# Kernel tuning notes

Measured on AMD Instinct MI355X. Metric: run time of the kernel, lower is better.

The kernel has to match this reference:

```python
import jax, jax.numpy as jnp
import numpy as np
import math

SCALED = True
SUBSEQUENT_MASK = True
B, SQ, SK, D, DV = 8, 2048, 2048, 1024, 1024


def _build_mask(query_lens, key_lens, sq, sk, causal):
    # (B, Sq, Sk) boolean validity mask: rows >= q_len and cols >= k_len are masked.
    qm = jnp.arange(sq)[None, :, None] < query_lens[:, None, None]
    km = jnp.arange(sk)[None, None, :] < key_lens[:, None, None]
    mask = qm & km
    if causal:
        mask = mask & (jnp.arange(sk)[None, None, :] <= jnp.arange(sq)[None, :, None])
    return mask


def _masked_softmax(scores, mask):
    # Stable masked softmax; fully-masked rows yield exactly 0 (matches the
    # original's NaN -> 0 replacement) without producing NaNs.
    neg = jnp.finfo(scores.dtype).min
    s = jnp.where(mask, scores, neg)
    m = jnp.max(s, axis=-1, keepdims=True)
    e = jnp.where(mask, jnp.exp(s - m), jnp.zeros((), scores.dtype))
    denom = jnp.sum(e, axis=-1, keepdims=True)
    return e / jnp.where(denom == 0, jnp.ones((), scores.dtype), denom)


def setup_inputs() -> dict:
    key = jax.random.key(0)
    kq, kk, kv, kql, kkl = jax.random.split(key, 5)
    return {
        "queries": jax.random.normal(kq, (B, SQ, D), dtype=jnp.float32),
        "keys": jax.random.normal(kk, (B, SK, D), dtype=jnp.float32),
        "values": jax.random.normal(kv, (B, SK, DV), dtype=jnp.float32),
        "query_lens": jax.random.randint(kql, (B,), 1, SQ + 1),
        "key_lens": jax.random.randint(kkl, (B,), 1, SK + 1),
    }


def reference(queries, keys, values, query_lens, key_lens):
    # scores: (B, Sq, Sk)
    scores = jnp.einsum("bqd,bkd->bqk", queries, keys)
    if SCALED:
        scores = scores / math.sqrt(queries.shape[2])
    mask = _build_mask(query_lens, key_lens, queries.shape[1], keys.shape[1], SUBSEQUENT_MASK)
    weights = _masked_softmax(scores, mask)
    context = jnp.einsum("bqk,bkv->bqv", weights, values)
    return (context, weights)
```

## Files before the change

kernel.cpp:

```cpp
#include <hip/hip_runtime.h>
#include <hip/hip_bf16.h>

#define B_   8
#define SQ_  2048
#define SK_  2048
#define D_   1024
#define DV_  1024

typedef __bf16 bf16;
typedef __attribute__((ext_vector_type(4))) __bf16 bf16x4;
typedef __attribute__((ext_vector_type(8))) __bf16 bf16x8;
typedef __attribute__((ext_vector_type(4))) float  f32x4;

typedef const __attribute__((address_space(1))) void* gptr1;
typedef __attribute__((address_space(3))) void*       lptr3;

__device__ __forceinline__ void gload16(const void* g, void* l) {
    __builtin_amdgcn_global_load_lds((gptr1)g, (lptr3)l, 16, 0, 0);
}

__global__ __launch_bounds__(256)
void convert_kernel(const float* __restrict__ A, const float* __restrict__ Bm,
                    bf16* __restrict__ dA, bf16* __restrict__ dB)
{
    const float* src = blockIdx.y ? Bm : A;
    bf16*        dst = blockIdx.y ? dB : dA;
    size_t i = ((size_t)blockIdx.x * 256 + threadIdx.x) * 8;
    float4 v0 = *(const float4*)(src + i);
    float4 v1 = *(const float4*)(src + i + 4);
    bf16x8 o = { (bf16)v0.x, (bf16)v0.y, (bf16)v0.z, (bf16)v0.w,
                 (bf16)v1.x, (bf16)v1.y, (bf16)v1.z, (bf16)v1.w };
    *(bf16x8*)(dst + i) = o;
}

__global__ __launch_bounds__(256)
void convVT_kernel(const float* __restrict__ V, bf16* __restrict__ VT)
{
    const int b  = blockIdx.z;
    const int k0 = blockIdx.x * 64;
    const int n0 = blockIdx.y * 64;
    __shared__ bf16 T[64][72];

    const int tid = threadIdx.x;
    #pragma unroll
    for (int i = 0; i < 4; ++i) {
        int s  = tid + i * 256;
        int r  = s >> 4;
        int c4 = (s & 15) << 2;
        float4 v = *(const float4*)(V + ((size_t)b * SK_ + (k0 + r)) * DV_ + n0 + c4);
        T[r][c4 + 0] = (bf16)v.x;
        T[r][c4 + 1] = (bf16)v.y;
        T[r][c4 + 2] = (bf16)v.z;
        T[r][c4 + 3] = (bf16)v.w;
    }
    __syncthreads();
    #pragma unroll
    for (int i = 0; i < 2; ++i) {
        int s  = tid + i * 256;
        int n  = s >> 3;
        int c8 = (s & 7) << 3;
        bf16x8 o;
        #pragma unroll
        for (int j = 0; j < 8; ++j) o[j] = T[c8 + j][n];
        *(bf16x8*)(VT + ((size_t)b * DV_ + (n0 + n)) * SK_ + k0 + c8) = o;
    }
}

__global__ __launch_bounds__(512, 4)
void scores_bf_kernel(const bf16* __restrict__ Qbf, const bf16* __restrict__ Kbf,
                      const int* __restrict__ qlens, const int* __restrict__ klens,
                      float* __restrict__ Wout)
{
    const int b  = blockIdx.z;
    const int q0 = blockIdx.y * 128;
    const int k0 = blockIdx.x * 128;
    if (k0 > q0 + 127) return;
    const int qlen = qlens[b], klen = klens[b];
    if (q0 >= qlen || k0 >= klen) return;

    __shared__ __align__(16) bf16 Qs[2][128][64];
    __shared__ __align__(16) bf16 Ks[2][128][64];

    const int tid  = threadIdx.x;
    const int lane = tid & 63;
    const int w    = tid >> 6;
    const int wq   = w >> 1, wk = w & 1;

    const bf16* Qb = Qbf + (size_t)b * SQ_ * D_ + (size_t)q0 * D_;
    const bf16* Kb = Kbf + (size_t)b * SK_ * D_ + (size_t)k0 * D_;

    const int r0 = tid >> 3;
    const int c0 = (tid & 7) << 3;

    auto stage = [&](int buf, int d0) {
        gload16(Qb + (size_t)r0 * D_ + d0 + c0,        &Qs[buf][r0][c0]);
        gload16(Qb + (size_t)(r0 + 64) * D_ + d0 + c0, &Qs[buf][r0 + 64][c0]);
        gload16(Kb + (size_t)r0 * D_ + d0 + c0,        &Ks[buf][r0][c0]);
        gload16(Kb + (size_t)(r0 + 64) * D_ + d0 + c0, &Ks[buf][r0 + 64][c0]);
    };

    f32x4 acc[2][4] = {};

    stage(0, 0);
    __syncthreads();

    for (int it = 0; it < 16; ++it) {
        const int cur = it & 1;
        if (it < 15) stage(cur ^ 1, (it + 1) * 64);
        #pragma unroll
        for (int kk = 0; kk < 2; ++kk) {
            const int koff = kk * 32 + ((lane >> 4) << 3);
            bf16x8 a[2], bb[4];
            #pragma unroll
            for (int m = 0; m < 2; ++m)
                a[m] = *(const bf16x8*)&Qs[cur][32 * wq + 16 * m + (lane & 15)][koff];
            #pragma unroll
            for (int n = 0; n < 4; ++n)
                bb[n] = *(const bf16x8*)&Ks[cur][64 * wk + 16 * n + (lane & 15)][koff];
            #pragma unroll
            for (int m = 0; m < 2; ++m)
                #pragma unroll
                for (int n = 0; n < 4; ++n)
                    acc[m][n] = __builtin_amdgcn_mfma_f32_16x16x32_bf16(a[m], bb[n], acc[m][n], 0, 0, 0);
        }
        __syncthreads();
    }

    float* Wb = Wout + (size_t)b * SQ_ * SK_;
    const int rb = q0 + 32 * wq + ((lane >> 4) << 2);
    const int cb = k0 + 64 * wk + (lane & 15);
    #pragma unroll
    for (int m = 0; m < 2; ++m)
        #pragma unroll
        for (int n = 0; n < 4; ++n)
            #pragma unroll
            for (int r = 0; r < 4; ++r)
                Wb[(size_t)(rb + 16 * m + r) * SK_ + (cb + 16 * n)] = acc[m][n][r] * 0.03125f;
}

__global__ __launch_bounds__(256)
void softmax_kernel(const int* __restrict__ qlens, const int* __restrict__ klens,
                    float* __restrict__ W, bf16* __restrict__ Wbf)
{
    const int bq = blockIdx.x;
    const int b  = bq >> 11;
    const int q  = bq & 2047;
    const int qlen = qlens[b], klen = klens[b];
    int kmax = 0;
    if (q < qlen) kmax = min(klen, q + 1);

    float4* row = (float4*)(W + (size_t)bq * SK_);
    const int tid = threadIdx.x;

    float4 x[2];
    float m = -INFINITY;
    #pragma unroll
    for (int i = 0; i < 2; ++i) {
        int v4 = tid + i * 256;
        int kb = v4 << 2;
        if (kb < kmax) x[i] = row[v4];
        else           x[i] = make_float4(-INFINITY, -INFINITY, -INFINITY, -INFINITY);
        float* xe = (float*)&x[i];
        #pragma unroll
        for (int e = 0; e < 4; ++e) {
            if (kb + e >= kmax) xe[e] = -INFINITY;
            m = fmaxf(m, xe[e]);
        }
    }
    #pragma unroll
    for (int off = 32; off > 0; off >>= 1) m = fmaxf(m, __shfl_xor(m, off, 64));
    __shared__ float red[4];
    if ((tid & 63) == 0) red[tid >> 6] = m;
    __syncthreads();
    m = fmaxf(fmaxf(red[0], red[1]), fmaxf(red[2], red[3]));
    __syncthreads();

    float sum = 0.f;
    #pragma unroll
    for (int i = 0; i < 2; ++i) {
        float* xe = (float*)&x[i];
        #pragma unroll
        for (int e = 0; e < 4; ++e) {
            float ev = (xe[e] == -INFINITY) ? 0.f : __expf(xe[e] - m);
            xe[e] = ev;
            sum += ev;
        }
    }
    #pragma unroll
    for (int off = 32; off > 0; off >>= 1) sum += __shfl_xor(sum, off, 64);
    if ((tid & 63) == 0) red[tid >> 6] = sum;
    __syncthreads();
    sum = red[0] + red[1] + red[2] + red[3];

    const float inv = (sum > 0.f) ? (1.f / sum) : 0.f;
    #pragma unroll
    for (int i = 0; i < 2; ++i) {
        float* xe = (float*)&x[i];
        float4 o = { xe[0] * inv, xe[1] * inv, xe[2] * inv, xe[3] * inv };
        row[tid + i * 256] = o;
        if (Wbf) {
            bf16x4 ob = { (bf16)o.x, (bf16)o.y, (bf16)o.z, (bf16)o.w };
            *(bf16x4*)(Wbf + (size_t)bq * SK_ + ((size_t)(tid + i * 256) << 2)) = ob;
        }
    }
}

__global__ __launch_bounds__(512, 4)
void context_bf_kernel(const bf16* __restrict__ Wbf, const bf16* __restrict__ VT,
                       const int* __restrict__ qlens, const int* __restrict__ klens,
                       float* __restrict__ Out)
{
    const int b  = blockIdx.z;
    const int q0 = blockIdx.y * 128;
    const int n0 = blockIdx.x * 128;
    const int tid  = threadIdx.x;
    const int qlen = qlens[b];

    float* Ob = Out + (size_t)b * SQ_ * DV_;
    if (q0 >= qlen) {
        float4 z = make_float4(0.f, 0.f, 0.f, 0.f);
        #pragma unroll
        for (int i = 0; i < 8; ++i) {
            int s  = tid + i * 512;
            int r  = s >> 5;
            int c4 = (s & 31) << 2;
            *(float4*)(Ob + (size_t)(q0 + r) * DV_ + n0 + c4) = z;
        }
        return;
    }

    const int klen = klens[b];
    const int kend = min(q0 + 128, (klen + 63) & ~63);
    const int nk   = kend >> 6;

    __shared__ __align__(16) bf16 Ws[2][128][64];
    __shared__ __align__(16) bf16 Vs[2][128][64];

    const int lane = tid & 63;
    const int w    = tid >> 6;
    const int wq   = w >> 1, wn = w & 1;

    const bf16* Wb = Wbf + (size_t)b * SQ_ * SK_ + (size_t)q0 * SK_;
    const bf16* Vb = VT  + (size_t)b * DV_ * SK_ + (size_t)n0 * SK_;

    const int r0 = tid >> 3;
    const int c0 = (tid & 7) << 3;

    auto stage = [&](int buf, int kk0) {
        gload16(Wb + (size_t)r0 * SK_ + kk0 + c0,        &Ws[buf][r0][c0]);
        gload16(Wb + (size_t)(r0 + 64) * SK_ + kk0 + c0, &Ws[buf][r0 + 64][c0]);
        gload16(Vb + (size_t)r0 * SK_ + kk0 + c0,        &Vs[buf][r0][c0]);
        gload16(Vb + (size_t)(r0 + 64) * SK_ + kk0 + c0, &Vs[buf][r0 + 64][c0]);
    };

    f32x4 acc[2][4] = {};

    stage(0, 0);
    __syncthreads();

    for (int it = 0; it < nk; ++it) {
        const int cur = it & 1;
        if (it + 1 < nk) stage(cur ^ 1, (it + 1) * 64);
        #pragma unroll
        for (int kk = 0; kk < 2; ++kk) {
            const int koff = kk * 32 + ((lane >> 4) << 3);
            bf16x8 a[2], bb[4];
            #pragma unroll
            for (int m = 0; m < 2; ++m)
                a[m] = *(const bf16x8*)&Ws[cur][32 * wq + 16 * m + (lane & 15)][koff];
            #pragma unroll
            for (int n = 0; n < 4; ++n)
                bb[n] = *(const bf16x8*)&Vs[cur][64 * wn + 16 * n + (lane & 15)][koff];
            #pragma unroll
            for (int m = 0; m < 2; ++m)
                #pragma unroll
                for (int n = 0; n < 4; ++n)
                    acc[m][n] = __builtin_amdgcn_mfma_f32_16x16x32_bf16(a[m], bb[n], acc[m][n], 0, 0, 0);
        }
        __syncthreads();
    }

    const int rb = q0 + 32 * wq + ((lane >> 4) << 2);
    const int cb = n0 + 64 * wn + (lane & 15);
    #pragma unroll
    for (int m = 0; m < 2; ++m)
        #pragma unroll
        for (int n = 0; n < 4; ++n)
            #pragma unroll
            for (int r = 0; r < 4; ++r)
                Ob[(size_t)(rb + 16 * m + r) * DV_ + (cb + 16 * n)] = acc[m][n][r];
}

__global__ __launch_bounds__(512, 4)
void scores_kernel(const float* __restrict__ Q, const float* __restrict__ K,
                   const int* __restrict__ qlens, const int* __restrict__ klens,
                   float* __restrict__ Wout)
{
    const int b  = blockIdx.z;
    const int q0 = blockIdx.y * 128;
    const int k0 = blockIdx.x * 128;
    if (k0 > q0 + 127) return;
    const int qlen = qlens[b], klen = klens[b];
    if (q0 >= qlen || k0 >= klen) return;

    __shared__ __align__(16) bf16 Qs[2][128][72];
    __shared__ __align__(16) bf16 Ks[2][128][72];

    const int tid  = threadIdx.x;
    const int lane = tid & 63;
    const int w    = tid >> 6;
    const int wq   = w >> 1, wk = w & 1;

    const float* Qb = Q + (size_t)b * SQ_ * D_;
    const float* Kb = K + (size_t)b * SK_ * D_;

    float4 qreg[4], kreg[4];
    int srow[4], sc4[4];
    #pragma unroll
    for (int i = 0; i < 4; ++i) {
        int s = tid + i * 512;
        srow[i] = s >> 4;
        sc4[i]  = (s & 15) << 2;
    }

    auto load_tile = [&](int d0) {
        #pragma unroll
        for (int i = 0; i < 4; ++i) {
            qreg[i] = *(const float4*)(Qb + (size_t)(q0 + srow[i]) * D_ + d0 + sc4[i]);
            kreg[i] = *(const float4*)(Kb + (size_t)(k0 + srow[i]) * D_ + d0 + sc4[i]);
        }
    };
    auto store_tile = [&](int buf) {
        #pragma unroll
        for (int i = 0; i < 4; ++i) {
            bf16x4 qb = { (bf16)qreg[i].x, (bf16)qreg[i].y, (bf16)qreg[i].z, (bf16)qreg[i].w };
            bf16x4 kb = { (bf16)kreg[i].x, (bf16)kreg[i].y, (bf16)kreg[i].z, (bf16)kreg[i].w };
            *(bf16x4*)&Qs[buf][srow[i]][sc4[i]] = qb;
            *(bf16x4*)&Ks[buf][srow[i]][sc4[i]] = kb;
        }
    };

    f32x4 acc[2][4] = {};
    load_tile(0);
    store_tile(0);
    __syncthreads();

    for (int it = 0; it < 16; ++it) {
        const int cur = it & 1;
        if (it < 15) load_tile((it + 1) * 64);
        #pragma unroll
        for (int kk = 0; kk < 2; ++kk) {
            const int koff = kk * 32 + ((lane >> 4) << 3);
            bf16x8 a[2], bb[4];
            #pragma unroll
            for (int m = 0; m < 2; ++m)
                a[m] = *(const bf16x8*)&Qs[cur][32 * wq + 16 * m + (lane & 15)][koff];
            #pragma unroll
            for (int n = 0; n < 4; ++n)
                bb[n] = *(const bf16x8*)&Ks[cur][64 * wk + 16 * n + (lane & 15)][koff];
            #pragma unroll
            for (int m = 0; m < 2; ++m)
                #pragma unroll
                for (int n = 0; n < 4; ++n)
                    acc[m][n] = __builtin_amdgcn_mfma_f32_16x16x32_bf16(a[m], bb[n], acc[m][n], 0, 0, 0);
        }
        if (it < 15) store_tile(1 - cur);
        __syncthreads();
    }

    float* Wb = Wout + (size_t)b * SQ_ * SK_;
    const int rb = q0 + 32 * wq + ((lane >> 4) << 2);
    const int cb = k0 + 64 * wk + (lane & 15);
    #pragma unroll
    for (int m = 0; m < 2; ++m)
        #pragma unroll
        for (int n = 0; n < 4; ++n)
            #pragma unroll
            for (int r = 0; r < 4; ++r)
                Wb[(size_t)(rb + 16 * m + r) * SK_ + (cb + 16 * n)] = acc[m][n][r] * 0.03125f;
}

__global__ __launch_bounds__(512, 4)
void context_kernel(const float* __restrict__ W, const float* __restrict__ V,
                    const int* __restrict__ klens, float* __restrict__ Out)
{
    const int b  = blockIdx.z;
    const int q0 = blockIdx.y * 128;
    const int n0 = blockIdx.x * 128;
    const int klen = klens[b];
    const int kend = min(q0 + 128, (klen + 63) & ~63);
    const int nk   = kend >> 6;

    __shared__ __align__(16) bf16 Ws[2][128][72];
    __shared__ __align__(16) bf16 Vs[2][128][72];

    const int tid  = threadIdx.x;
    const int lane = tid & 63;
    const int w    = tid >> 6;
    const int wq   = w >> 1, wn = w & 1;

    const float* Wb = W + (size_t)b * SQ_ * SK_;
    const float* Vb = V + (size_t)b * SK_ * DV_;

    float4 wreg[4];
    float  vreg[2][8];
    int srow[4], sc4[4], vn[2], voct[2];
    #pragma unroll
    for (int i = 0; i < 4; ++i) {
        int s = tid + i * 512;
        srow[i] = s >> 4;
        sc4[i]  = (s & 15) << 2;
    }
    #pragma unroll
    for (int i = 0; i < 2; ++i) {
        int t = tid + i * 512;
        vn[i]   = t & 127;
        voct[i] = t >> 7;
    }

    auto load_tile = [&](int kk0) {
        #pragma unroll
        for (int i = 0; i < 4; ++i)
            wreg[i] = *(const float4*)(Wb + (size_t)(q0 + srow[i]) * SK_ + kk0 + sc4[i]);
        #pragma unroll
        for (int i = 0; i < 2; ++i)
            #pragma unroll
            for (int j = 0; j < 8; ++j)
                vreg[i][j] = Vb[(size_t)(kk0 + voct[i] * 8 + j) * DV_ + n0 + vn[i]];
    };
    auto store_tile = [&](int buf) {
        #pragma unroll
        for (int i = 0; i < 4; ++i) {
            bf16x4 wb = { (bf16)wreg[i].x, (bf16)wreg[i].y, (bf16)wreg[i].z, (bf16)wreg[i].w };
            *(bf16x4*)&Ws[buf][srow[i]][sc4[i]] = wb;
        }
        #pragma unroll
        for (int i = 0; i < 2; ++i) {
            bf16x8 vb = { (bf16)vreg[i][0], (bf16)vreg[i][1], (bf16)vreg[i][2], (bf16)vreg[i][3],
                          (bf16)vreg[i][4], (bf16)vreg[i][5], (bf16)vreg[i][6], (bf16)vreg[i][7] };
            *(bf16x8*)&Vs[buf][vn[i]][voct[i] * 8] = vb;
        }
    };

    f32x4 acc[2][4] = {};
    load_tile(0);
    store_tile(0);
    __syncthreads();

    for (int it = 0; it < nk; ++it) {
        const int cur = it & 1;
        if (it + 1 < nk) load_tile((it + 1) * 64);
        #pragma unroll
        for (int kk = 0; kk < 2; ++kk) {
            const int koff = kk * 32 + ((lane >> 4) << 3);
            bf16x8 a[2], bb[4];
            #pragma unroll
            for (int m = 0; m < 2; ++m)
                a[m] = *(const bf16x8*)&Ws[cur][32 * wq + 16 * m + (lane & 15)][koff];
            #pragma unroll
            for (int n = 0; n < 4; ++n)
                bb[n] = *(const bf16x8*)&Vs[cur][64 * wn + 16 * n + (lane & 15)][koff];
            #pragma unroll
            for (int m = 0; m < 2; ++m)
                #pragma unroll
                for (int n = 0; n < 4; ++n)
                    acc[m][n] = __builtin_amdgcn_mfma_f32_16x16x32_bf16(a[m], bb[n], acc[m][n], 0, 0, 0);
        }
        if (it + 1 < nk) store_tile(1 - cur);
        __syncthreads();
    }

    float* Ob = Out + (size_t)b * SQ_ * DV_;
    const int rb = q0 + 32 * wq + ((lane >> 4) << 2);
    const int cb = n0 + 64 * wn + (lane & 15);
    #pragma unroll
    for (int m = 0; m < 2; ++m)
        #pragma unroll
        for (int n = 0; n < 4; ++n)
            #pragma unroll
            for (int r = 0; r < 4; ++r)
                Ob[(size_t)(rb + 16 * m + r) * DV_ + (cb + 16 * n)] = acc[m][n][r];
}

extern "C" void kernel_launch(void* const* d_in, const int* in_sizes, int n_in,
                              void* d_out, int out_size, void* d_ws, size_t ws_size,
                              hipStream_t stream) {
    (void)in_sizes; (void)n_in; (void)out_size;
    const float* Q     = (const float*)d_in[0];
    const float* K     = (const float*)d_in[1];
    const float* V     = (const float*)d_in[2];
    const int*   qlens = (const int*)d_in[3];
    const int*   klens = (const int*)d_in[4];

    float* ctx = (float*)d_out;
    float* wts = ctx + (size_t)B_ * SQ_ * DV_;

    const size_t nQ = (size_t)B_ * SQ_ * D_;
    const size_t nK = (size_t)B_ * SK_ * D_;
    const size_t nV = (size_t)B_ * SK_ * DV_;
    const size_t nW = (size_t)B_ * SQ_ * SK_;
    const size_t ws_need = (nQ + nK + nV + nW) * sizeof(bf16);

    if (d_ws && ws_size >= ws_need) {
        bf16* qbf = (bf16*)d_ws;
        bf16* kbf = qbf + nQ;
        bf16* vbt = kbf + nK;
        bf16* wbf = vbt + nV;

        convert_kernel<<<dim3((unsigned)(nQ / (256 * 8)), 2), 256, 0, stream>>>(Q, K, qbf, kbf);
        convVT_kernel<<<dim3(SK_ / 64, DV_ / 64, B_), 256, 0, stream>>>(V, vbt);

        dim3 g1(SK_ / 128, SQ_ / 128, B_);
        scores_bf_kernel<<<g1, 512, 0, stream>>>(qbf, kbf, qlens, klens, wts);

        softmax_kernel<<<dim3(B_ * SQ_), 256, 0, stream>>>(qlens, klens, wts, wbf);

        dim3 g3(DV_ / 128, SQ_ / 128, B_);
        context_bf_kernel<<<g3, 512, 0, stream>>>(wbf, vbt, qlens, klens, ctx);
    } else {
        dim3 g1(SK_ / 128, SQ_ / 128, B_);
        scores_kernel<<<g1, 512, 0, stream>>>(Q, K, qlens, klens, wts);

        softmax_kernel<<<dim3(B_ * SQ_), 256, 0, stream>>>(qlens, klens, wts, (bf16*)nullptr);

        dim3 g3(DV_ / 128, SQ_ / 128, B_);
        context_kernel<<<g3, 512, 0, stream>>>(wts, V, klens, ctx);
    }
}
```

Measured before the change: 492.8 us.

## Fuse exp into QK kernel and defer softmax normalization to context epilogue

The separate scores and softmax passes are replaced by an attnP kernel that computes QK^T tiles, applies the mask and exp without subtracting a row max, writes unnormalized bf16 probabilities, and accumulates row sums via atomics. A normW kernel then writes the normalized fp32 weights from the bf16 buffer, and the context kernel scales its output by the inverse row sum. The goal is to cut the fp32 score write and read round trip and the separate softmax pass. In exchange, the QK grid becomes 512 blocks of 64-row tiles that loop over key tiles, which lowers parallelism and reloads Q for each key tile. Dropping the max subtraction risks overflow for inputs with large scores, and the fp32 weights are now rounded through bf16.

```diff
diff --git a/kernel.cpp b/kernel.cpp
--- a/kernel.cpp
+++ b/kernel.cpp
@@ -21,8 +21,15 @@
 
 __global__ __launch_bounds__(256)
 void convert_kernel(const float* __restrict__ A, const float* __restrict__ Bm,
-                    bf16* __restrict__ dA, bf16* __restrict__ dB)
-{
+                    bf16* __restrict__ dA, bf16* __restrict__ dB,
+                    float* __restrict__ rowsumG)
+{
+    if (rowsumG && blockIdx.y == 0 && blockIdx.x < 8) {
+        int idx = blockIdx.x * 256 + threadIdx.x;
+        float4 z = make_float4(0.f, 0.f, 0.f, 0.f);
+        ((float4*)rowsumG)[idx * 2 + 0] = z;
+        ((float4*)rowsumG)[idx * 2 + 1] = z;
+    }
     const float* src = blockIdx.y ? Bm : A;
     bf16*        dst = blockIdx.y ? dB : dA;
     size_t i = ((size_t)blockIdx.x * 256 + threadIdx.x) * 8;
@@ -67,9 +74,247 @@
 }
 
 __global__ __launch_bounds__(512, 4)
-void scores_bf_kernel(const bf16* __restrict__ Qbf, const bf16* __restrict__ Kbf,
-                      const int* __restrict__ qlens, const int* __restrict__ klens,
-                      float* __restrict__ Wout)
+void attnP_kernel(const bf16* __restrict__ Qbf, const bf16* __restrict__ Kbf,
+                  const int* __restrict__ qlens, const int* __restrict__ klens,
+                  bf16* __restrict__ Wbf, float* __restrict__ rowsumG)
+{
+    const int v    = blockIdx.x & 255;
+    const int inst = blockIdx.x >> 8;
+    const int b    = v & 7;
+    const int s    = v >> 3;
+    const int qs   = inst ? (31 - s) : s;
+    const int par  = inst;
+    const int q0   = qs * 64;
+    const int qlen = qlens[b], klen = klens[b];
+    if (q0 >= qlen) return;
+
+    const int ncols  = min(klen, q0 + 64);
+    const int ktiles = (ncols + 127) >> 7;
+
+    __shared__ __align__(16) bf16 Qs[2][64][64];
+    __shared__ __align__(16) bf16 Ks[2][128][64];
+    __shared__ float rowsum[64];
+
+    const int tid  = threadIdx.x;
+    const int lane = tid & 63;
+    const int w    = tid >> 6;
+
+    if (tid < 64) rowsum[tid] = 0.f;
+
+    const bf16* Qb = Qbf + ((size_t)b * SQ_ + q0) * (size_t)D_;
+    const bf16* Kb = Kbf + (size_t)b * SK_ * (size_t)D_;
+    bf16* Wrow0 = Wbf + ((size_t)b * SQ_ + q0) * SK_;
+
+    const int r0 = tid >> 3;
+    const int c0 = (tid & 7) << 3;
+    const int g  = lane >> 4;
+    const int cl = lane & 15;
+
+    for (int kt = par; kt < ktiles; kt += 2) {
+        const bf16* Kt = Kb + (size_t)(kt * 128) * (size_t)D_;
+        gload16(Qb + (size_t)r0 * D_ + c0,        &Qs[0][r0][c0]);
+        gload16(Kt + (size_t)r0 * D_ + c0,        &Ks[0][r0][c0]);
+        gload16(Kt + (size_t)(r0 + 64) * D_ + c0, &Ks[0][r0 + 64][c0]);
+        __syncthreads();
+
+        f32x4 acc[4] = {};
+        for (int dc = 0; dc < 16; ++dc) {
+            const int cur = dc & 1;
+            if (dc < 15) {
+                const int d1 = (dc + 1) * 64;
+                gload16(Qb + (size_t)r0 * D_ + d1 + c0,        &Qs[cur ^ 1][r0][c0]);
+                gload16(Kt + (size_t)r0 * D_ + d1 + c0,        &Ks[cur ^ 1][r0][c0]);
+                gload16(Kt + (size_t)(r0 + 64) * D_ + d1 + c0, &Ks[cur ^ 1][r0 + 64][c0]);
+            }
+            #pragma unroll
+            for (int st = 0; st < 2; ++st) {
+                const int koff = st * 32 + (g << 3);
+                bf16x8 bb = *(const bf16x8*)&Ks[cur][16 * w + cl][koff];
+                #pragma unroll
+                for (int t = 0; t < 4; ++t) {
+                    bf16x8 a = *(const bf16x8*)&Qs[cur][16 * t + cl][koff];
+                    acc[t] = __builtin_amdgcn_mfma_f32_16x16x32_bf16(a, bb, acc[t], 0, 0, 0);
+                }
+            }
+            __syncthreads();
+        }
+
+        const int colg = kt * 128 + 16 * w + cl;
+        #pragma unroll
+        for (int t = 0; t < 4; ++t) {
+            #pragma unroll
+            for (int r = 0; r < 4; ++r) {
+                const int rl   = 16 * t + 4 * g + r;
+                const int rowg = q0 + rl;
+                float e = 0.f;
+                if (rowg < qlen && colg <= rowg && colg < klen)
+                    e = __expf(acc[t][r] * 0.03125f);
+                Wrow0[(size_t)rl * SK_ + colg] = (bf16)e;
+                float esum = e;
+                esum += __shfl_xor(esum, 1, 64);
+                esum += __shfl_xor(esum, 2, 64);
+                esum += __shfl_xor(esum, 4, 64);
+                esum += __shfl_xor(esum, 8, 64);
+                if (cl == 0) atomicAdd(&rowsum[rl], esum);
+            }
+        }
+    }
+
+    __syncthreads();
+    if (tid < 64) {
+        float sv = rowsum[tid];
+        if (sv > 0.f) atomicAdd(&rowsumG[(size_t)b * SQ_ + q0 + tid], sv);
+    }
+}
+
+__global__ __launch_bounds__(512)
+void normW_kernel(const int* __restrict__ qlens, const int* __restrict__ klens,
+                  const float* __restrict__ rowsumG, bf16* __restrict__ Wbf,
+                  float* __restrict__ W, float* __restrict__ invG)
+{
+    const int b  = blockIdx.y;
+    const int q0 = blockIdx.x * 64;
+    const int qlen = qlens[b], klen = klens[b];
+    const int tid = threadIdx.x;
+    float* Wb = W + ((size_t)b * SQ_ + q0) * SK_;
+
+    if (q0 >= qlen) {
+        float4 z = make_float4(0.f, 0.f, 0.f, 0.f);
+        float4* wf = (float4*)Wb;
+        #pragma unroll
+        for (int i = 0; i < 64; ++i) wf[tid + i * 512] = z;
+        float4* bfp = (float4*)(Wbf + ((size_t)b * SQ_ + q0) * SK_);
+        #pragma unroll
+        for (int i = 0; i < 32; ++i) bfp[tid + i * 512] = z;
+        if (tid < 64) invG[(size_t)b * SQ_ + q0 + tid] = 0.f;
+        return;
+    }
+
+    const int ncols = min(klen, q0 + 64);
+    const int kendB = ((ncols + 127) >> 7) << 7;
+
+    __shared__ float invS[64];
+    if (tid < 64) {
+        float sv = rowsumG[(size_t)b * SQ_ + q0 + tid];
+        float iv = (sv > 0.f) ? (1.f / sv) : 0.f;
+        invS[tid] = iv;
+        invG[(size_t)b * SQ_ + q0 + tid] = iv;
+    }
+    __syncthreads();
+
+    const int r  = tid >> 3;
+    const int c8 = tid & 7;
+    const float iv = invS[r];
+    const bf16* Erow = Wbf + ((size_t)b * SQ_ + q0 + r) * SK_;
+    float* Wrow = Wb + (size_t)r * SK_;
+    for (int j = 0; j < 64; ++j) {
+        int col = (c8 + j * 8) << 2;
+        float4 o;
+        if (col < kendB) {
+            bf16x4 e4 = *(const bf16x4*)&Erow[col];
+            o = make_float4((float)e4[0] * iv, (float)e4[1] * iv,
+                            (float)e4[2] * iv, (float)e4[3] * iv);
+        } else {
+            o = make_float4(0.f, 0.f, 0.f, 0.f);
+        }
+        *(float4*)&Wrow[col] = o;
+    }
+}
+
+__global__ __launch_bounds__(512, 4)
+void context_bf_kernel(const bf16* __restrict__ Wbf, const bf16* __restrict__ VT,
+                       const int* __restrict__ qlens, const int* __restrict__ klens,
+                       const float* __restrict__ invG, float* __restrict__ Out)
+{
+    const int b  = blockIdx.z;
+    const int q0 = blockIdx.y * 128;
+    const int n0 = blockIdx.x * 128;
+    const int tid  = threadIdx.x;
+    const int qlen = qlens[b];
+
+    float* Ob = Out + (size_t)b * SQ_ * DV_;
+    if (q0 >= qlen) {
+        float4 z = make_float4(0.f, 0.f, 0.f, 0.f);
+        #pragma unroll
+        for (int i = 0; i < 8; ++i) {
+            int s  = tid + i * 512;
+            int r  = s >> 5;
+            int c4 = (s & 31) << 2;
+            *(float4*)(Ob + (size_t)(q0 + r) * DV_ + n0 + c4) = z;
+        }
+        return;
+    }
+
+    const int klen = klens[b];
+    const int kend = min(q0 + 128, (klen + 63) & ~63);
+    const int nk   = kend >> 6;
+
+    __shared__ __align__(16) bf16 Ws[2][128][64];
+    __shared__ __align__(16) bf16 Vs[2][128][64];
+
+    const int lane = tid & 63;
+    const int w    = tid >> 6;
+    const int wq   = w >> 1, wn = w & 1;
+
+    const bf16* Wb = Wbf + (size_t)b * SQ_ * SK_ + (size_t)q0 * SK_;
+    const bf16* Vb = VT  + (size_t)b * DV_ * SK_ + (size_t)n0 * SK_;
+
+    const int r0 = tid >> 3;
+    const int c0 = (tid & 7) << 3;
+
+    auto stage = [&](int buf, int kk0) {
+        gload16(Wb + (size_t)r0 * SK_ + kk0 + c0,        &Ws[buf][r0][c0]);
+        gload16(Wb + (size_t)(r0 + 64) * SK_ + kk0 + c0, &Ws[buf][r0 + 64][c0]);
+        gload16(Vb + (size_t)r0 * SK_ + kk0 + c0,        &Vs[buf][r0][c0]);
+        gload16(Vb + (size_t)(r0 + 64) * SK_ + kk0 + c0, &Vs[buf][r0 + 64][c0]);
+    };
+
+    f32x4 acc[2][4] = {};
+
+    stage(0, 0);
+    __syncthreads();
+
+    for (int it = 0; it < nk; ++it) {
+        const int cur = it & 1;
+        if (it + 1 < nk) stage(cur ^ 1, (it + 1) * 64);
+        #pragma unroll
+        for (int kk = 0; kk < 2; ++kk) {
+            const int koff = kk * 32 + ((lane >> 4) << 3);
+            bf16x8 a[2], bb[4];
+            #pragma unroll
+            for (int m = 0; m < 2; ++m)
+                a[m] = *(const bf16x8*)&Ws[cur][32 * wq + 16 * m + (lane & 15)][koff];
+            #pragma unroll
+            for (int n = 0; n < 4; ++n)
+                bb[n] = *(const bf16x8*)&Vs[cur][64 * wn + 16 * n + (lane & 15)][koff];
+            #pragma unroll
+            for (int m = 0; m < 2; ++m)
+                #pragma unroll
+                for (int n = 0; n < 4; ++n)
+                    acc[m][n] = __builtin_amdgcn_mfma_f32_16x16x32_bf16(a[m], bb[n], acc[m][n], 0, 0, 0);
+        }
+        __syncthreads();
+    }
+
+    const float* invB = invG + (size_t)b * SQ_;
+    const int rb = q0 + 32 * wq + ((lane >> 4) << 2);
+    const int cb = n0 + 64 * wn + (lane & 15);
+    #pragma unroll
+    for (int m = 0; m < 2; ++m) {
+        #pragma unroll
+        for (int r = 0; r < 4; ++r) {
+            const float iv = invB[rb + 16 * m + r];
+            #pragma unroll
+            for (int n = 0; n < 4; ++n)
+                Ob[(size_t)(rb + 16 * m + r) * DV_ + (cb + 16 * n)] = acc[m][n][r] * iv;
+        }
+    }
+}
+
+__global__ __launch_bounds__(512, 4)
+void scores_kernel(const float* __restrict__ Q, const float* __restrict__ K,
+                   const int* __restrict__ qlens, const int* __restrict__ klens,
+                   float* __restrict__ Wout)
 {
     const int b  = blockIdx.z;
     const int q0 = blockIdx.y * 128;
@@ -78,35 +323,51 @@
     const int qlen = qlens[b], klen = klens[b];
     if (q0 >= qlen || k0 >= klen) return;
 
-    __shared__ __align__(16) bf16 Qs[2][128][64];
-    __shared__ __align__(16) bf16 Ks[2][128][64];
+    __shared__ __align__(16) bf16 Qs[2][128][72];
+    __shared__ __align__(16) bf16 Ks[2][128][72];
 
     const int tid  = threadIdx.x;
     const int lane = tid & 63;
     const int w    = tid >> 6;
     const int wq   = w >> 1, wk = w & 1;
 
-    const bf16* Qb = Qbf + (size_t)b * SQ_ * D_ + (size_t)q0 * D_;
-    const bf16* Kb = Kbf + (size_t)b * SK_ * D_ + (size_t)k0 * D_;
-
-    const int r0 = tid >> 3;
-    const int c0 = (tid & 7) << 3;
-
-    auto stage = [&](int buf, int d0) {
-        gload16(Qb + (size_t)r0 * D_ + d0 + c0,        &Qs[buf][r0][c0]);
-        gload16(Qb + (size_t)(r0 + 64) * D_ + d0 + c0, &Qs[buf][r0 + 64][c0]);
-        gload16(Kb + (size_t)r0 * D_ + d0 + c0,        &Ks[buf][r0][c0]);
-        gload16(Kb + (size_t)(r0 + 64) * D_ + d0 + c0, &Ks[buf][r0 + 64][c0]);
+    const float* Qb = Q + (size_t)b * SQ_ * D_;
+    const float* Kb = K + (size_t)b * SK_ * D_;
+
+    float4 qreg[4], kreg[4];
+    int srow[4], sc4[4];
+    #pragma unroll
+    for (int i = 0; i < 4; ++i) {
+        int s = tid + i * 512;
+        srow[i] = s >> 4;
+        sc4[i]  = (s & 15) << 2;
+    }
+
+    auto load_tile = [&](int d0) {
+        #pragma unroll
+        for (int i = 0; i < 4; ++i) {
+            qreg[i] = *(const float4*)(Qb + (size_t)(q0 + srow[i]) * D_ + d0 + sc4[i]);
+            kreg[i] = *(const float4*)(Kb + (size_t)(k0 + srow[i]) * D_ + d0 + sc4[i]);
+        }
     };
+    auto store_tile = [&](int buf) {
+        #pragma unroll
+        for (int i = 0; i < 4; ++i) {
+            bf16x4 qb = { (bf16)qreg[i].x, (bf16)qreg[i].y, (bf16)qreg[i].z, (bf16)qreg[i].w };
+            bf16x4 kb = { (bf16)kreg[i].x, (bf16)kreg[i].y, (bf16)kreg[i].z, (bf16)kreg[i].w };
+            *(bf16x4*)&Qs[buf][srow[i]][sc4[i]] = qb;
+            *(bf16x4*)&Ks[buf][srow[i]][sc4[i]] = kb;
+        }
+    };
 
     f32x4 acc[2][4] = {};
-
-    stage(0, 0);
+    load_tile(0);
+    store_tile(0);
     __syncthreads();
 
     for (int it = 0; it < 16; ++it) {
         const int cur = it & 1;
-        if (it < 15) stage(cur ^ 1, (it + 1) * 64);
+        if (it < 15) load_tile((it + 1) * 64);
         #pragma unroll
         for (int kk = 0; kk < 2; ++kk) {
             const int koff = kk * 32 + ((lane >> 4) << 3);
@@ -123,6 +384,7 @@
                 for (int n = 0; n < 4; ++n)
                     acc[m][n] = __builtin_amdgcn_mfma_f32_16x16x32_bf16(a[m], bb[n], acc[m][n], 0, 0, 0);
         }
+        if (it < 15) store_tile(1 - cur);
         __syncthreads();
     }
 
@@ -140,7 +402,7 @@
 
 __global__ __launch_bounds__(256)
 void softmax_kernel(const int* __restrict__ qlens, const int* __restrict__ klens,
-                    float* __restrict__ W, bf16* __restrict__ Wbf)
+                    float* __restrict__ W)
 {
     const int bq = blockIdx.x;
     const int b  = bq >> 11;
@@ -198,186 +460,7 @@
         float* xe = (float*)&x[i];
         float4 o = { xe[0] * inv, xe[1] * inv, xe[2] * inv, xe[3] * inv };
         row[tid + i * 256] = o;
-        if (Wbf) {
-            bf16x4 ob = { (bf16)o.x, (bf16)o.y, (bf16)o.z, (bf16)o.w };
-            *(bf16x4*)(Wbf + (size_t)bq * SK_ + ((size_t)(tid + i * 256) << 2)) = ob;
-        }
-    }
-}
-
-__global__ __launch_bounds__(512, 4)
-void context_bf_kernel(const bf16* __restrict__ Wbf, const bf16* __restrict__ VT,
-                       const int* __restrict__ qlens, const int* __restrict__ klens,
-                       float* __restrict__ Out)
-{
-    const int b  = blockIdx.z;
-    const int q0 = blockIdx.y * 128;
-    const int n0 = blockIdx.x * 128;
-    const int tid  = threadIdx.x;
-    const int qlen = qlens[b];
-
-    float* Ob = Out + (size_t)b * SQ_ * DV_;
-    if (q0 >= qlen) {
-        float4 z = make_float4(0.f, 0.f, 0.f, 0.f);
-        #pragma unroll
-        for (int i = 0; i < 8; ++i) {
-            int s  = tid + i * 512;
-            int r  = s >> 5;
-            int c4 = (s & 31) << 2;
-            *(float4*)(Ob + (size_t)(q0 + r) * DV_ + n0 + c4) = z;
-        }
-        return;
-    }
-
-    const int klen = klens[b];
-    const int kend = min(q0 + 128, (klen + 63) & ~63);
-    const int nk   = kend >> 6;
-
-    __shared__ __align__(16) bf16 Ws[2][128][64];
-    __shared__ __align__(16) bf16 Vs[2][128][64];
-
-    const int lane = tid & 63;
-    const int w    = tid >> 6;
-    const int wq   = w >> 1, wn = w & 1;
-
-    const bf16* Wb = Wbf + (size_t)b * SQ_ * SK_ + (size_t)q0 * SK_;
-    const bf16* Vb = VT  + (size_t)b * DV_ * SK_ + (size_t)n0 * SK_;
-
-    const int r0 = tid >> 3;
-    const int c0 = (tid & 7) << 3;
-
-    auto stage = [&](int buf, int kk0) {
-        gload16(Wb + (size_t)r0 * SK_ + kk0 + c0,        &Ws[buf][r0][c0]);
-        gload16(Wb + (size_t)(r0 + 64) * SK_ + kk0 + c0, &Ws[buf][r0 + 64][c0]);
-        gload16(Vb + (size_t)r0 * SK_ + kk0 + c0,        &Vs[buf][r0][c0]);
-        gload16(Vb + (size_t)(r0 + 64) * SK_ + kk0 + c0, &Vs[buf][r0 + 64][c0]);
-    };
-
-    f32x4 acc[2][4] = {};
-
-    stage(0, 0);
-    __syncthreads();
-
-    for (int it = 0; it < nk; ++it) {
-        const int cur = it & 1;
-        if (it + 1 < nk) stage(cur ^ 1, (it + 1) * 64);
-        #pragma unroll
-        for (int kk = 0; kk < 2; ++kk) {
-            const int koff = kk * 32 + ((lane >> 4) << 3);
-            bf16x8 a[2], bb[4];
-            #pragma unroll
-            for (int m = 0; m < 2; ++m)
-                a[m] = *(const bf16x8*)&Ws[cur][32 * wq + 16 * m + (lane & 15)][koff];
-            #pragma unroll
-            for (int n = 0; n < 4; ++n)
-                bb[n] = *(const bf16x8*)&Vs[cur][64 * wn + 16 * n + (lane & 15)][koff];
-            #pragma unroll
-            for (int m = 0; m < 2; ++m)
-                #pragma unroll
-                for (int n = 0; n < 4; ++n)
-                    acc[m][n] = __builtin_amdgcn_mfma_f32_16x16x32_bf16(a[m], bb[n], acc[m][n], 0, 0, 0);
-        }
-        __syncthreads();
-    }
-
-    const int rb = q0 + 32 * wq + ((lane >> 4) << 2);
-    const int cb = n0 + 64 * wn + (lane & 15);
-    #pragma unroll
-    for (int m = 0; m < 2; ++m)
-        #pragma unroll
-        for (int n = 0; n < 4; ++n)
-            #pragma unroll
-            for (int r = 0; r < 4; ++r)
-                Ob[(size_t)(rb + 16 * m + r) * DV_ + (cb + 16 * n)] = acc[m][n][r];
-}
-
-__global__ __launch_bounds__(512, 4)
-void scores_kernel(const float* __restrict__ Q, const float* __restrict__ K,
-                   const int* __restrict__ qlens, const int* __restrict__ klens,
-                   float* __restrict__ Wout)
-{
-    const int b  = blockIdx.z;
-    const int q0 = blockIdx.y * 128;
-    const int k0 = blockIdx.x * 128;
-    if (k0 > q0 + 127) return;
-    const int qlen = qlens[b], klen = klens[b];
-    if (q0 >= qlen || k0 >= klen) return;
-
-    __shared__ __align__(16) bf16 Qs[2][128][72];
-    __shared__ __align__(16) bf16 Ks[2][128][72];
-
-    const int tid  = threadIdx.x;
-    const int lane = tid & 63;
-    const int w    = tid >> 6;
-    const int wq   = w >> 1, wk = w & 1;
-
-    const float* Qb = Q + (size_t)b * SQ_ * D_;
-    const float* Kb = K + (size_t)b * SK_ * D_;
-
-    float4 qreg[4], kreg[4];
-    int srow[4], sc4[4];
-    #pragma unroll
-    for (int i = 0; i < 4; ++i) {
-        int s = tid + i * 512;
-        srow[i] = s >> 4;
-        sc4[i]  = (s & 15) << 2;
-    }
-
-    auto load_tile = [&](int d0) {
-        #pragma unroll
-        for (int i = 0; i < 4; ++i) {
-            qreg[i] = *(const float4*)(Qb + (size_t)(q0 + srow[i]) * D_ + d0 + sc4[i]);
-            kreg[i] = *(const float4*)(Kb + (size_t)(k0 + srow[i]) * D_ + d0 + sc4[i]);
-        }
-    };
-    auto store_tile = [&](int buf) {
-        #pragma unroll
-        for (int i = 0; i < 4; ++i) {
-            bf16x4 qb = { (bf16)qreg[i].x, (bf16)qreg[i].y, (bf16)qreg[i].z, (bf16)qreg[i].w };
-            bf16x4 kb = { (bf16)kreg[i].x, (bf16)kreg[i].y, (bf16)kreg[i].z, (bf16)kreg[i].w };
-            *(bf16x4*)&Qs[buf][srow[i]][sc4[i]] = qb;
-            *(bf16x4*)&Ks[buf][srow[i]][sc4[i]] = kb;
-        }
-    };
-
-    f32x4 acc[2][4] = {};
-    load_tile(0);
-    store_tile(0);
-    __syncthreads();
-
-    for (int it = 0; it < 16; ++it) {
-        const int cur = it & 1;
-        if (it < 15) load_tile((it + 1) * 64);
-        #pragma unroll
-        for (int kk = 0; kk < 2; ++kk) {
-            const int koff = kk * 32 + ((lane >> 4) << 3);
-            bf16x8 a[2], bb[4];
-            #pragma unroll
-            for (int m = 0; m < 2; ++m)
-                a[m] = *(const bf16x8*)&Qs[cur][32 * wq + 16 * m + (lane & 15)][koff];
-            #pragma unroll
-            for (int n = 0; n < 4; ++n)
-                bb[n] = *(const bf16x8*)&Ks[cur][64 * wk + 16 * n + (lane & 15)][koff];
-            #pragma unroll
-            for (int m = 0; m < 2; ++m)
-                #pragma unroll
-                for (int n = 0; n < 4; ++n)
-                    acc[m][n] = __builtin_amdgcn_mfma_f32_16x16x32_bf16(a[m], bb[n], acc[m][n], 0, 0, 0);
-        }
-        if (it < 15) store_tile(1 - cur);
-        __syncthreads();
-    }
-
-    float* Wb = Wout + (size_t)b * SQ_ * SK_;
-    const int rb = q0 + 32 * wq + ((lane >> 4) << 2);
-    const int cb = k0 + 64 * wk + (lane & 15);
-    #pragma unroll
-    for (int m = 0; m < 2; ++m)
-        #pragma unroll
-        for (int n = 0; n < 4; ++n)
-            #pragma unroll
-            for (int r = 0; r < 4; ++r)
-                Wb[(size_t)(rb + 16 * m + r) * SK_ + (cb + 16 * n)] = acc[m][n][r] * 0.03125f;
+    }
 }
 
 __global__ __launch_bounds__(512, 4)
@@ -499,29 +582,31 @@
     const size_t nK = (size_t)B_ * SK_ * D_;
     const size_t nV = (size_t)B_ * SK_ * DV_;
     const size_t nW = (size_t)B_ * SQ_ * SK_;
-    const size_t ws_need = (nQ + nK + nV + nW) * sizeof(bf16);
+    const size_t nS = (size_t)B_ * SQ_;
+    const size_t ws_need = (nQ + nK + nV + nW) * sizeof(bf16) + nS * 2 * sizeof(float);
 
     if (d_ws && ws_size >= ws_need) {
-        bf16* qbf = (bf16*)d_ws;
-        bf16* kbf = qbf + nQ;
-        bf16* vbt = kbf + nK;
-        bf16* wbf = vbt + nV;
-
-        convert_kernel<<<dim3((unsigned)(nQ / (256 * 8)), 2), 256, 0, stream>>>(Q, K, qbf, kbf);
+        bf16*  qbf = (bf16*)d_ws;
+        bf16*  kbf = qbf + nQ;
+        bf16*  vbt = kbf + nK;
+        bf16*  wbf = vbt + nV;
+        float* rowsumG = (float*)(wbf + nW);
+        float* invG    = rowsumG + nS;
+
+        convert_kernel<<<dim3((unsigned)(nQ / (256 * 8)), 2), 256, 0, stream>>>(Q, K, qbf, kbf, rowsumG);
         convVT_kernel<<<dim3(SK_ / 64, DV_ / 64, B_), 256, 0, stream>>>(V, vbt);
 
-        dim3 g1(SK_ / 128, SQ_ / 128, B_);
-        scores_bf_kernel<<<g1, 512, 0, stream>>>(qbf, kbf, qlens, klens, wts);
-
-        softmax_kernel<<<dim3(B_ * SQ_), 256, 0, stream>>>(qlens, klens, wts, wbf);
+        attnP_kernel<<<dim3(512), 512, 0, stream>>>(qbf, kbf, qlens, klens, wbf, rowsumG);
+
+        normW_kernel<<<dim3(SQ_ / 64, B_), 512, 0, stream>>>(qlens, klens, rowsumG, wbf, wts, invG);
 
         dim3 g3(DV_ / 128, SQ_ / 128, B_);
-        context_bf_kernel<<<g3, 512, 0, stream>>>(wbf, vbt, qlens, klens, ctx);
+        context_bf_kernel<<<g3, 512, 0, stream>>>(wbf, vbt, qlens, klens, invG, ctx);
     } else {
         dim3 g1(SK_ / 128, SQ_ / 128, B_);
         scores_kernel<<<g1, 512, 0, stream>>>(Q, K, qlens, klens, wts);
 
-        softmax_kernel<<<dim3(B_ * SQ_), 256, 0, stream>>>(qlens, klens, wts, (bf16*)nullptr);
+        softmax_kernel<<<dim3(B_ * SQ_), 256, 0, stream>>>(qlens, klens, wts);
 
         dim3 g3(DV_ / 128, SQ_ / 128, B_);
         context_kernel<<<g3, 512, 0, stream>>>(wts, V, klens, ctx);
```

After: 550.7 us. 11.7% more time.
